# Optimization experiments

Hardware: AMD Instinct MI355X
Metric: run time of the kernel (lower is better)

The kernel has to match this reference:

```python
import jax, jax.numpy as jnp
import numpy as np

B, Q, T, C = 2, 300, 25, 256
NH, NL, NP = 8, 4, 4
DFF = 1024
HD = C // NH
SHAPES = [(128, 128), (64, 64), (32, 32), (16, 16)]  # (H_l, W_l) per level
S = sum(h * w for h, w in SHAPES)
LQ = Q * T


def setup_inputs() -> dict:
    key = jax.random.key(0)
    ks = jax.random.split(key, 16)
    rn = lambda k, shape, s=0.02: jax.random.normal(k, shape, jnp.float32) * s
    starts = np.cumsum([0] + [h * w for h, w in SHAPES[:-1]])
    return {
        "tgt_text": jax.random.normal(ks[0], (B, Q, T, C), jnp.float32),
        "query_pos_text": jax.random.normal(ks[1], (B, Q, T, C), jnp.float32),
        "reference_points": jax.random.uniform(ks[2], (B, LQ, NL, 2), jnp.float32),
        "src": jax.random.normal(ks[3], (B, S, C), jnp.float32),
        "src_spatial_shapes": jnp.array(SHAPES, jnp.int32),
        "level_start_index": jnp.array(starts, jnp.int32),
        "in_proj_w": rn(ks[4], (3 * C, C)), "in_proj_b": jnp.zeros((3 * C,), jnp.float32),
        "out_proj_w": rn(ks[5], (C, C)), "out_proj_b": jnp.zeros((C,), jnp.float32),
        "ln1_g": jnp.ones((C,), jnp.float32), "ln1_b": jnp.zeros((C,), jnp.float32),
        "samp_off_w": rn(ks[6], (NH * NL * NP * 2, C)), "samp_off_b": rn(ks[7], (NH * NL * NP * 2,), 0.5),
        "aw_w": rn(ks[8], (NH * NL * NP, C)), "aw_b": jnp.zeros((NH * NL * NP,), jnp.float32),
        "vp_w": rn(ks[9], (C, C)), "vp_b": jnp.zeros((C,), jnp.float32),
        "op_w": rn(ks[10], (C, C)), "op_b": jnp.zeros((C,), jnp.float32),
        "ln2_g": jnp.ones((C,), jnp.float32), "ln2_b": jnp.zeros((C,), jnp.float32),
        "ffn1_w": rn(ks[11], (DFF, C)), "ffn1_b": jnp.zeros((DFF,), jnp.float32),
        "ffn2_w": rn(ks[12], (C, DFF)), "ffn2_b": jnp.zeros((C,), jnp.float32),
        "ln3_g": jnp.ones((C,), jnp.float32), "ln3_b": jnp.zeros((C,), jnp.float32),
    }


def _ln(x, g, b):
    m = jnp.mean(x, axis=-1, keepdims=True)
    v = jnp.var(x, axis=-1, keepdims=True)
    return (x - m) / jnp.sqrt(v + 1e-5) * g + b


def _self_attn(tgt, pos, in_proj_w, in_proj_b, out_proj_w, out_proj_b):
    # torch nn.MultiheadAttention math: q,k carry pos, v is raw tgt
    qk = (tgt + pos).reshape(B * Q, T, C)
    x = tgt.reshape(B * Q, T, C)
    Wq, Wk, Wv = jnp.split(in_proj_w, 3, axis=0)
    bq, bk, bv = jnp.split(in_proj_b, 3, axis=0)
    heads = lambda t: t.reshape(B * Q, T, NH, HD).transpose(0, 2, 1, 3)
    q = heads(qk @ Wq.T + bq)
    k = heads(qk @ Wk.T + bk)
    v = heads(x @ Wv.T + bv)
    attn = jax.nn.softmax(jnp.einsum("bhqd,bhkd->bhqk", q, k) / jnp.sqrt(jnp.float32(HD)), axis=-1)
    o = jnp.einsum("bhqk,bhkd->bhqd", attn, v).transpose(0, 2, 1, 3).reshape(B * Q, T, C)
    return (o @ out_proj_w.T + out_proj_b).reshape(B, Q, T, C)


def _ms_deform_attn(query, reference_points, src, shapes, samp_off_w, samp_off_b, aw_w, aw_b, vp_w, vp_b, op_w, op_b):
    # query: [B, LQ, C]; src: [B, S, C]
    value = (src @ vp_w.T + vp_b).reshape(B, S, NH, HD)
    off = (query @ samp_off_w.T + samp_off_b).reshape(B, LQ, NH, NL, NP, 2)
    aw = jax.nn.softmax((query @ aw_w.T + aw_b).reshape(B, LQ, NH, NL * NP), axis=-1)
    aw = aw.reshape(B, LQ, NH, NL, NP)
    # normalizer is (W_l, H_l)
    norm = jnp.array([[w, h] for (h, w) in shapes], jnp.float32)
    loc = reference_points[:, :, None, :, None, :] + off / norm[None, None, None, :, None, :]
    starts = np.cumsum([0] + [h * w for h, w in shapes])
    accum = jnp.zeros((B, NH, LQ, HD), jnp.float32)
    for l, (Hl, Wl) in enumerate(shapes):
        vl = value[:, starts[l]:starts[l] + Hl * Wl].transpose(0, 2, 1, 3)  # [B,NH,HW,HD]
        # grid_sample align_corners=False pixel coords
        xl = (loc[:, :, :, l, :, 0] * Wl - 0.5).transpose(0, 2, 1, 3).reshape(B, NH, LQ * NP)
        yl = (loc[:, :, :, l, :, 1] * Hl - 0.5).transpose(0, 2, 1, 3).reshape(B, NH, LQ * NP)
        x0 = jnp.floor(xl); y0 = jnp.floor(yl)
        wx1 = xl - x0; wy1 = yl - y0
        x0i = x0.astype(jnp.int32); y0i = y0.astype(jnp.int32)
        samp = jnp.zeros((B, NH, LQ * NP, HD), jnp.float32)
        for dx, dy, w in ((0, 0, (1 - wx1) * (1 - wy1)), (1, 0, wx1 * (1 - wy1)),
                          (0, 1, (1 - wx1) * wy1), (1, 1, wx1 * wy1)):
            xi = x0i + dx; yi = y0i + dy
            valid = (xi >= 0) & (xi < Wl) & (yi >= 0) & (yi < Hl)
            lin = jnp.clip(yi, 0, Hl - 1) * Wl + jnp.clip(xi, 0, Wl - 1)
            g = jnp.take_along_axis(vl, lin[..., None], axis=2)  # [B,NH,LQ*NP,HD]
            samp = samp + g * (w * valid)[..., None]
        samp = samp.reshape(B, NH, LQ, NP, HD)
        awl = aw[:, :, :, l, :].transpose(0, 2, 1, 3)  # [B,NH,LQ,NP]
        accum = accum + jnp.sum(samp * awl[..., None], axis=3)
    out = accum.transpose(0, 2, 1, 3).reshape(B, LQ, C)
    return out @ op_w.T + op_b


def reference(tgt_text, query_pos_text, reference_points, src, src_spatial_shapes, level_start_index,
              in_proj_w, in_proj_b, out_proj_w, out_proj_b, ln1_g, ln1_b,
              samp_off_w, samp_off_b, aw_w, aw_b, vp_w, vp_b, op_w, op_b, ln2_g, ln2_b,
              ffn1_w, ffn1_b, ffn2_w, ffn2_b, ln3_g, ln3_b):
    shapes = [tuple(int(v) for v in row) for row in np.asarray(src_spatial_shapes)]  # static
    # --- intra-text self-attention ---
    tgt2 = _self_attn(tgt_text, query_pos_text, in_proj_w, in_proj_b, out_proj_w, out_proj_b)
    tgt = _ln(tgt_text + tgt2, ln1_g, ln1_b)
    # --- multi-scale deformable cross-attention ---
    query = (tgt + query_pos_text).reshape(B, LQ, C)
    cross = _ms_deform_attn(query, reference_points, src, shapes,
                            samp_off_w, samp_off_b, aw_w, aw_b, vp_w, vp_b, op_w, op_b)
    tgt = _ln(tgt + cross.reshape(B, Q, T, C), ln2_g, ln2_b)
    # --- FFN ---
    ffn = jax.nn.relu(tgt @ ffn1_w.T + ffn1_b) @ ffn2_w.T + ffn2_b
    return _ln(tgt + ffn, ln3_g, ln3_b)
```

## Files before the change

### kernel.cpp

```cpp
#include <hip/hip_runtime.h>
#include <cstddef>

#define B_ 2
#define Q_ 300
#define T_ 25
#define C_ 256
#define NH_ 8
#define NL_ 4
#define NP_ 4
#define HD_ 32
#define DFF_ 1024
#define LQ_ (Q_ * T_)
#define NTOK_ (B_ * LQ_)
#define S_ 21760
#define BS_ (B_ * S_)

typedef __bf16 bf16x8 __attribute__((ext_vector_type(8)));
typedef float floatx4 __attribute__((ext_vector_type(4)));
typedef unsigned short ushort_t;

__device__ __forceinline__ unsigned pack_bf16(float x, float y) {
    unsigned ux = __float_as_uint(x) + 0x8000u;
    unsigned uy = __float_as_uint(y) + 0x8000u;
    return (ux >> 16) | (uy & 0xFFFF0000u);
}
__device__ __forceinline__ ushort_t f2bf_s(float x) {
    return (ushort_t)((__float_as_uint(x) + 0x8000u) >> 16);
}
__device__ __forceinline__ float bf2f(ushort_t u) {
    return __uint_as_float((unsigned)u << 16);
}

#define WOFF_IP   0
#define WOFF_OUT  196608
#define WOFF_VP   262144
#define WOFF_SO   327680
#define WOFF_AW   393216
#define WOFF_OP   425984
#define WOFF_F1   491520
#define WOFF_F2   753664
#define WTOTAL    1015808

__global__ __launch_bounds__(256) void convw_kernel(
    const float* __restrict__ ipw, const float* __restrict__ outw,
    const float* __restrict__ vpw, const float* __restrict__ sampw,
    const float* __restrict__ aww, const float* __restrict__ opw,
    const float* __restrict__ f1w, const float* __restrict__ f2w,
    ushort_t* __restrict__ dst)
{
    long long g = ((long long)blockIdx.x * 256 + threadIdx.x) * 8;
    if (g >= WTOTAL) return;
    const float* src; long long off;
    if      (g < WOFF_OUT) { src = ipw;   off = WOFF_IP; }
    else if (g < WOFF_VP)  { src = outw;  off = WOFF_OUT; }
    else if (g < WOFF_SO)  { src = vpw;   off = WOFF_VP; }
    else if (g < WOFF_AW)  { src = sampw; off = WOFF_SO; }
    else if (g < WOFF_OP)  { src = aww;   off = WOFF_AW; }
    else if (g < WOFF_F1)  { src = opw;   off = WOFF_OP; }
    else if (g < WOFF_F2)  { src = f1w;   off = WOFF_F1; }
    else                   { src = f2w;   off = WOFF_F2; }
    const float4* s4 = (const float4*)(src + (g - off));
    float4 a = s4[0], b = s4[1];
    uint4 o;
    o.x = pack_bf16(a.x, a.y); o.y = pack_bf16(a.z, a.w);
    o.z = pack_bf16(b.x, b.y); o.w = pack_bf16(b.z, b.w);
    *(uint4*)(dst + g) = o;
}

#define GBN 128
#define GBK 64
#define LDA_S 72

template<int AMODE, int OUTMODE, int GBMT>
__global__ __launch_bounds__(256) void gemm_w(
    const void* __restrict__ Av, const float* __restrict__ A2,
    const ushort_t* __restrict__ W,
    const float* __restrict__ bias, const float* __restrict__ bias2, int N1,
    void* __restrict__ Cv, long long partStride,
    int M, int N, int K, int kChunk, int ldc, int relu)
{
    constexpr int LA = GBMT / 16;
    constexpr int LB = 8;
    constexpr int WM = GBMT / 2;
    constexpr int NI = WM / 16;

    __shared__ unsigned short SH[GBMT * LDA_S + GBN * LDA_S];
    unsigned short* Asl = SH;
    unsigned short* Bsl = SH + GBMT * LDA_S;

    const int m0 = blockIdx.x * GBMT;
    if (m0 >= M) return;
    const int n0 = blockIdx.y * GBN;
    const int z  = blockIdx.z;
    const int kbeg = z * kChunk;
    const int kend = min(K, kbeg + kChunk);

    const int t  = threadIdx.x;
    const int wid  = t >> 6;
    const int lane = t & 63;
    const int wm = (wid >> 1) * WM;
    const int wn = (wid & 1) * 64;
    const int fm = lane & 15;
    const int fq = (lane >> 4) * 8;

    const bool addA2 = (AMODE == 1) && (n0 < N1);

    floatx4 acc[NI][4];
    #pragma unroll
    for (int i = 0; i < NI; ++i)
        #pragma unroll
        for (int j = 0; j < 4; ++j)
            acc[i][j] = (floatx4){0.f, 0.f, 0.f, 0.f};

    float4 pa[LA];
    uint2  pab[LA];
    uint2  pwb[LB];
    const float* Af = (const float*)Av;
    const ushort_t* Ab = (const ushort_t*)Av;

    auto load_tiles = [&](int k0) {
        #pragma unroll
        for (int i = 0; i < LA; ++i) {
            int idx = t + 256 * i;
            int row = idx >> 4;
            int c4  = (idx & 15) * 4;
            int gm = m0 + row;
            if constexpr (AMODE == 2) {
                uint2 v = {0u, 0u};
                if (gm < M) v = *(const uint2*)(Ab + (size_t)gm * K + k0 + c4);
                pab[i] = v;
            } else {
                float4 v = make_float4(0.f, 0.f, 0.f, 0.f);
                if (gm < M) {
                    v = *(const float4*)(Af + (size_t)gm * K + k0 + c4);
                    if constexpr (AMODE == 1) {
                        if (addA2) {
                            float4 v2 = *(const float4*)(A2 + (size_t)gm * K + k0 + c4);
                            v.x += v2.x; v.y += v2.y; v.z += v2.z; v.w += v2.w;
                        }
                    }
                }
                pa[i] = v;
            }
        }
        #pragma unroll
        for (int i = 0; i < LB; ++i) {
            int idx = t + 256 * i;
            int row = idx >> 4;
            int c4  = (idx & 15) * 4;
            pwb[i] = *(const uint2*)(W + (size_t)(n0 + row) * K + k0 + c4);
        }
    };

    load_tiles(kbeg);
    for (int k0 = kbeg; k0 < kend; k0 += GBK) {
        #pragma unroll
        for (int i = 0; i < LA; ++i) {
            int idx = t + 256 * i;
            int row = idx >> 4;
            int c4  = (idx & 15) * 4;
            if constexpr (AMODE == 2) {
                *(uint2*)&Asl[row * LDA_S + c4] = pab[i];
            } else {
                uint2 p;
                p.x = pack_bf16(pa[i].x, pa[i].y);
                p.y = pack_bf16(pa[i].z, pa[i].w);
                *(uint2*)&Asl[row * LDA_S + c4] = p;
            }
        }
        #pragma unroll
        for (int i = 0; i < LB; ++i) {
            int idx = t + 256 * i;
            int row = idx >> 4;
            int c4  = (idx & 15) * 4;
            *(uint2*)&Bsl[row * LDA_S + c4] = pwb[i];
        }
        __syncthreads();
        if (k0 + GBK < kend) load_tiles(k0 + GBK);

        #pragma unroll
        for (int kk = 0; kk < 2; ++kk) {
            bf16x8 af[NI], bfr[4];
            #pragma unroll
            for (int i = 0; i < NI; ++i)
                af[i] = *(const bf16x8*)&Asl[(wm + i * 16 + fm) * LDA_S + kk * 32 + fq];
            #pragma unroll
            for (int j = 0; j < 4; ++j)
                bfr[j] = *(const bf16x8*)&Bsl[(wn + j * 16 + fm) * LDA_S + kk * 32 + fq];

            #pragma unroll
            for (int i = 0; i < NI; ++i)
                #pragma unroll
                for (int j = 0; j < 4; ++j)
                    acc[i][j] = __builtin_amdgcn_mfma_f32_16x16x32_bf16(af[i], bfr[j], acc[i][j], 0, 0, 0);
        }
        __syncthreads();
    }

    float* Cf = (float*)Cv + (long long)z * partStride;
    ushort_t* Cb = (ushort_t*)Cv;
    const int cr = (lane >> 4) * 4;
    const int cc = lane & 15;

    if constexpr (OUTMODE == 0) {
        #pragma unroll
        for (int j = 0; j < 4; ++j) {
            int gn = n0 + wn + j * 16 + cc;
            float bia = 0.f;
            if (z == 0) bia = (bias2 && gn >= N1) ? bias2[gn - N1] : bias[gn];
            #pragma unroll
            for (int i = 0; i < NI; ++i)
                #pragma unroll
                for (int r = 0; r < 4; ++r) {
                    int gm = m0 + wm + i * 16 + cr + r;
                    if (gm < M) {
                        float v = acc[i][j][r] + bia;
                        if (relu) v = fmaxf(v, 0.f);
                        Cf[(size_t)gm * ldc + gn] = v;
                    }
                }
        }
    } else {
        unsigned short* epi = SH + wid * (WM * 64);
        #pragma unroll
        for (int j = 0; j < 4; ++j) {
            int gn = n0 + wn + j * 16 + cc;
            float bia = (bias2 && gn >= N1) ? bias2[gn - N1] : bias[gn];
            #pragma unroll
            for (int i = 0; i < NI; ++i)
                #pragma unroll
                for (int r = 0; r < 4; ++r) {
                    float v = acc[i][j][r] + bia;
                    if (relu) v = fmaxf(v, 0.f);
                    epi[(i * 16 + cr + r) * 64 + j * 16 + cc] = f2bf_s(v);
                }
        }
        #pragma unroll
        for (int pass = 0; pass < WM / 8; ++pass) {
            int lr = pass * 8 + (lane >> 3);
            int gm = m0 + wm + lr;
            uint4 vv = *(const uint4*)&epi[lr * 64 + (lane & 7) * 8];
            if (gm < M) {
                if constexpr (OUTMODE == 1) {
                    *(uint4*)&Cb[(size_t)gm * ldc + n0 + wn + (lane & 7) * 8] = vv;
                } else {
                    int bb = gm >= S_;
                    int s  = gm - bb * S_;
                    int gh = n0 + wn + (lane & 7) * 8;
                    *(uint4*)&Cb[(((size_t)(bb * 8 + (gh >> 5))) * S_ + s) * 32 + (gh & 31)] = vv;
                }
            }
        }
    }
}

__global__ __launch_bounds__(64) void attn_kernel(
    const ushort_t* __restrict__ qkv,
    ushort_t* __restrict__ o)
{
    int sh = blockIdx.x;
    int s = sh >> 3, h = sh & 7;
    __shared__ float qs[T_][HD_], ks[T_][HD_], vs[T_][HD_];
    int t = threadIdx.x;

    for (int idx = t; idx < T_ * HD_; idx += 64) {
        int i = idx >> 5, d = idx & 31;
        size_t base = ((size_t)(s * T_ + i)) * 768 + h * HD_ + d;
        qs[i][d] = bf2f(qkv[base]);
        ks[i][d] = bf2f(qkv[base + 256]);
        vs[i][d] = bf2f(qkv[base + 512]);
    }
    __syncthreads();

    if (t < T_) {
        float sc[T_];
        float mx = -1e30f;
        #pragma unroll
        for (int j = 0; j < T_; ++j) {
            float dot = 0.f;
            #pragma unroll
            for (int d = 0; d < HD_; ++d) dot += qs[t][d] * ks[j][d];
            sc[j] = dot * 0.17677669529663687f;
            mx = fmaxf(mx, sc[j]);
        }
        float sum = 0.f;
        #pragma unroll
        for (int j = 0; j < T_; ++j) { sc[j] = __expf(sc[j] - mx); sum += sc[j]; }
        float inv = 1.f / sum;
        float out[HD_];
        #pragma unroll
        for (int d = 0; d < HD_; ++d) out[d] = 0.f;
        for (int j = 0; j < T_; ++j) {
            float p = sc[j] * inv;
            #pragma unroll
            for (int d = 0; d < HD_; ++d) out[d] += p * vs[j][d];
        }
        size_t ob = ((size_t)(s * T_ + t)) * C_ + h * HD_;
        #pragma unroll
        for (int d = 0; d < HD_; ++d) o[ob + d] = f2bf_s(out[d]);
    }
}

__global__ __launch_bounds__(256) void ln4_kernel(
    const float* x, const float* r,
    int nparts, long long rstride,
    const float* __restrict__ g, const float* __restrict__ b,
    float* out, const float* __restrict__ pos,
    float* qout)
{
    const int wave = threadIdx.x >> 6;
    const int lane = threadIdx.x & 63;
    const int tok = blockIdx.x * 4 + wave;
    const size_t base = (size_t)tok * C_ + lane * 4;

    float4 v = *(const float4*)(x + base);
    for (int p = 0; p < nparts; ++p) {
        float4 rv = *(const float4*)(r + base + (long long)p * rstride);
        v.x += rv.x; v.y += rv.y; v.z += rv.z; v.w += rv.w;
    }
    float s  = v.x + v.y + v.z + v.w;
    float ss = v.x * v.x + v.y * v.y + v.z * v.z + v.w * v.w;
    #pragma unroll
    for (int m = 32; m; m >>= 1) {
        s  += __shfl_xor(s, m);
        ss += __shfl_xor(ss, m);
    }
    float mean = s * (1.f / 256.f);
    float var  = ss * (1.f / 256.f) - mean * mean;
    float rstd = rsqrtf(var + 1e-5f);

    float4 gv = *(const float4*)(g + lane * 4);
    float4 bv = *(const float4*)(b + lane * 4);
    float4 y;
    y.x = (v.x - mean) * rstd * gv.x + bv.x;
    y.y = (v.y - mean) * rstd * gv.y + bv.y;
    y.z = (v.z - mean) * rstd * gv.z + bv.z;
    y.w = (v.w - mean) * rstd * gv.w + bv.w;
    *(float4*)(out + base) = y;
    if (qout) {
        float4 pv = *(const float4*)(pos + base);
        float4 q;
        q.x = y.x + pv.x; q.y = y.y + pv.y; q.z = y.z + pv.z; q.w = y.w + pv.w;
        *(float4*)(qout + base) = q;
    }
}

#define DCHUNK_ 118
__global__ __launch_bounds__(256) void deform_kernel(
    const ushort_t* __restrict__ value,
    const float* __restrict__ d12,
    const float* __restrict__ refpts,
    ushort_t* __restrict__ out)
{
    const int bi    = blockIdx.x;
    const int xcd   = bi & 7;
    const int yy    = bi >> 3;
    const int combo = xcd + 8 * (yy & 1);
    const int chunk = yy >> 1;
    const int h     = combo & 7;
    const int b     = combo >> 3;

    __shared__ float tls[64][60];

    const int tid = threadIdx.x;
    const int t0  = chunk * 64;

    #pragma unroll
    for (int i = 0; i < 2; ++i) {
        int idx  = tid + 256 * i;
        int trow = idx >> 3;
        int c4   = (idx & 7) * 4;
        int tl   = min(t0 + trow, LQ_ - 1);
        float4 v;
        v.x = __builtin_nontemporal_load(d12 + (size_t)(b * LQ_ + tl) * 384 + h * 32 + c4 + 0);
        v.y = __builtin_nontemporal_load(d12 + (size_t)(b * LQ_ + tl) * 384 + h * 32 + c4 + 1);
        v.z = __builtin_nontemporal_load(d12 + (size_t)(b * LQ_ + tl) * 384 + h * 32 + c4 + 2);
        v.w = __builtin_nontemporal_load(d12 + (size_t)(b * LQ_ + tl) * 384 + h * 32 + c4 + 3);
        *(float4*)&tls[trow][c4] = v;
    }
    {
        int trow = tid >> 2;
        int c4   = (tid & 3) * 4;
        int tl   = min(t0 + trow, LQ_ - 1);
        float4 v;
        v.x = __builtin_nontemporal_load(d12 + (size_t)(b * LQ_ + tl) * 384 + 256 + h * 16 + c4 + 0);
        v.y = __builtin_nontemporal_load(d12 + (size_t)(b * LQ_ + tl) * 384 + 256 + h * 16 + c4 + 1);
        v.z = __builtin_nontemporal_load(d12 + (size_t)(b * LQ_ + tl) * 384 + 256 + h * 16 + c4 + 2);
        v.w = __builtin_nontemporal_load(d12 + (size_t)(b * LQ_ + tl) * 384 + 256 + h * 16 + c4 + 3);
        *(float4*)&tls[trow][32 + c4] = v;
    }
    if (tid < 128) {
        int trow = tid >> 1;
        int c4   = (tid & 1) * 4;
        int tl   = min(t0 + trow, LQ_ - 1);
        float4 v;
        v.x = __builtin_nontemporal_load(refpts + (size_t)(b * LQ_ + tl) * 8 + c4 + 0);
        v.y = __builtin_nontemporal_load(refpts + (size_t)(b * LQ_ + tl) * 8 + c4 + 1);
        v.z = __builtin_nontemporal_load(refpts + (size_t)(b * LQ_ + tl) * 8 + c4 + 2);
        v.w = __builtin_nontemporal_load(refpts + (size_t)(b * LQ_ + tl) * 8 + c4 + 3);
        *(float4*)&tls[trow][48 + c4] = v;
    }
    __syncthreads();

    if (tid < 64) {
        float lg[16];
        float mx = -1e30f;
        #pragma unroll
        for (int i = 0; i < 16; ++i) { lg[i] = tls[tid][32 + i]; mx = fmaxf(mx, lg[i]); }
        float sum = 0.f;
        #pragma unroll
        for (int i = 0; i < 16; ++i) { lg[i] = __expf(lg[i] - mx); sum += lg[i]; }
        float inv = 1.f / sum;
        #pragma unroll
        for (int i = 0; i < 16; ++i) tls[tid][32 + i] = lg[i] * inv;
    }
    __syncthreads();

    const int wave = tid >> 6;
    const int lane = tid & 63;
    const int ti   = lane >> 2;
    const int d8   = (lane & 3) * 8;
    const int row  = wave * 16 + ti;

    int tl = t0 + row;
    const bool active = (tl < LQ_);
    tl = min(tl, LQ_ - 1);
    const int tok = b * LQ_ + tl;

    const int HW[4]     = {128, 64, 32, 16};
    const int starts[4] = {0, 16384, 20480, 21504};

    const ushort_t* vplane = value + (size_t)combo * ((size_t)S_ * HD_) + d8;
    const float* trow = tls[row];

    float accv[8];
    #pragma unroll
    for (int i = 0; i < 8; ++i) accv[i] = 0.f;

    #pragma unroll
    for (int l = 0; l < 4; ++l) {
        const int Hl = HW[l], Wl = HW[l];
        float rx = trow[48 + l * 2 + 0];
        float ry = trow[48 + l * 2 + 1];
        const ushort_t* vbase = vplane + (size_t)starts[l] * HD_;
        #pragma unroll
        for (int p = 0; p < 4; ++p) {
            float ox = trow[l * 8 + p * 2 + 0];
            float oy = trow[l * 8 + p * 2 + 1];
            float aww = trow[32 + l * 4 + p];
            float xl = rx * (float)Wl + ox - 0.5f;
            float yl = ry * (float)Hl + oy - 0.5f;
            float x0f = floorf(xl), y0f = floorf(yl);
            int x0 = (int)x0f, y0 = (int)y0f;
            float wx1 = xl - x0f, wy1 = yl - y0f;
            float wx0 = 1.f - wx1, wy0 = 1.f - wy1;

            #pragma unroll
            for (int c = 0; c < 4; ++c) {
                int dx = c & 1, dy = c >> 1;
                int xi = x0 + dx, yi = y0 + dy;
                float w = (dx ? wx1 : wx0) * (dy ? wy1 : wy0);
                bool valid = (xi >= 0) & (xi < Wl) & (yi >= 0) & (yi < Hl);
                int xc = min(max(xi, 0), Wl - 1);
                int yc = min(max(yi, 0), Hl - 1);
                float wc = (valid ? w : 0.f) * aww;
                uint4 raw = *(const uint4*)(vbase + (size_t)(yc * Wl + xc) * HD_);
                accv[0] += __uint_as_float((raw.x & 0xFFFFu) << 16) * wc;
                accv[1] += __uint_as_float(raw.x & 0xFFFF0000u) * wc;
                accv[2] += __uint_as_float((raw.y & 0xFFFFu) << 16) * wc;
                accv[3] += __uint_as_float(raw.y & 0xFFFF0000u) * wc;
                accv[4] += __uint_as_float((raw.z & 0xFFFFu) << 16) * wc;
                accv[5] += __uint_as_float(raw.z & 0xFFFF0000u) * wc;
                accv[6] += __uint_as_float((raw.w & 0xFFFFu) << 16) * wc;
                accv[7] += __uint_as_float(raw.w & 0xFFFF0000u) * wc;
            }
        }
    }
    if (active) {
        uint4 po;
        po.x = pack_bf16(accv[0], accv[1]);
        po.y = pack_bf16(accv[2], accv[3]);
        po.z = pack_bf16(accv[4], accv[5]);
        po.w = pack_bf16(accv[6], accv[7]);
        *(uint4*)(out + (size_t)tok * C_ + h * HD_ + d8) = po;
    }
}

extern "C" void kernel_launch(void* const* d_in, const int* in_sizes, int n_in,
                              void* d_out, int out_size, void* d_ws, size_t ws_size,
                              hipStream_t stream) {
    const float* tgt_text = (const float*)d_in[0];
    const float* pos      = (const float*)d_in[1];
    const float* refpts   = (const float*)d_in[2];
    const float* src      = (const float*)d_in[3];
    const float* in_proj_w  = (const float*)d_in[6];
    const float* in_proj_b  = (const float*)d_in[7];
    const float* out_proj_w = (const float*)d_in[8];
    const float* out_proj_b = (const float*)d_in[9];
    const float* ln1_g = (const float*)d_in[10];
    const float* ln1_b = (const float*)d_in[11];
    const float* samp_off_w = (const float*)d_in[12];
    const float* samp_off_b = (const float*)d_in[13];
    const float* aw_w = (const float*)d_in[14];
    const float* aw_b = (const float*)d_in[15];
    const float* vp_w = (const float*)d_in[16];
    const float* vp_b = (const float*)d_in[17];
    const float* op_w = (const float*)d_in[18];
    const float* op_b = (const float*)d_in[19];
    const float* ln2_g = (const float*)d_in[20];
    const float* ln2_b = (const float*)d_in[21];
    const float* ffn1_w = (const float*)d_in[22];
    const float* ffn1_b = (const float*)d_in[23];
    const float* ffn2_w = (const float*)d_in[24];
    const float* ffn2_b = (const float*)d_in[25];
    const float* ln3_g = (const float*)d_in[26];
    const float* ln3_b = (const float*)d_in[27];

    const long long NC = (long long)NTOK_ * C_;
    float* ws = (float*)d_ws;
    float* A    = ws;
    float* Bq   = ws + NC;
    float* Creg = ws + 2 * NC;
    float* D12  = Creg + (long long)NTOK_ * DFF_;
    float* E    = D12 + (long long)NTOK_ * 384;
    float* F    = E + NC;
    ushort_t* wb = (ushort_t*)(F + NC);

    ushort_t* qkv  = (ushort_t*)Creg;
    ushort_t* valt = (ushort_t*)Creg + (size_t)NTOK_ * 768;

    const int MB64P  = 240;
    const int MB128P = 120;
    const int MBV64  = BS_ / 64;

    convw_kernel<<<496, 256, 0, stream>>>(in_proj_w, out_proj_w, vp_w, samp_off_w,
                                          aw_w, op_w, ffn1_w, ffn2_w, wb);
    gemm_w<1, 1, 64><<<dim3(MB64P, 6, 1), 256, 0, stream>>>(tgt_text, pos, wb + WOFF_IP,
        in_proj_b, nullptr, 512, qkv, 0, NTOK_, 768, 256, 256, 768, 0);
    gemm_w<0, 2, 64><<<dim3(MBV64, 2, 1), 256, 0, stream>>>(src, nullptr, wb + WOFF_VP,
        vp_b, nullptr, 0, valt, 0, BS_, 256, 256, 256, 0, 0);
    attn_kernel<<<B_ * Q_ * NH_, 64, 0, stream>>>(qkv, (ushort_t*)E);
    gemm_w<2, 0, 64><<<dim3(MB64P, 2, 2), 256, 0, stream>>>(E, nullptr, wb + WOFF_OUT,
        out_proj_b, nullptr, 0, ws, NC, NTOK_, 256, 256, 128, 256, 0);
    ln4_kernel<<<NTOK_ / 4, 256, 0, stream>>>(tgt_text, ws, 2, NC,
                                              ln1_g, ln1_b, A, pos, Bq);
    gemm_w<0, 0, 64><<<dim3(MB64P, 3, 1), 256, 0, stream>>>(Bq, nullptr, wb + WOFF_SO,
        samp_off_b, aw_b, 256, D12, 0, NTOK_, 384, 256, 256, 384, 0);
    deform_kernel<<<8 * 2 * DCHUNK_, 256, 0, stream>>>(valt, D12, refpts, (ushort_t*)E);
    gemm_w<2, 0, 64><<<dim3(MB64P, 2, 2), 256, 0, stream>>>(E, nullptr, wb + WOFF_OP,
        op_b, nullptr, 0, Creg, NC, NTOK_, 256, 256, 128, 256, 0);
    ln4_kernel<<<NTOK_ / 4, 256, 0, stream>>>(A, Creg, 2, NC,
                                              ln2_g, ln2_b, A, nullptr, nullptr);
    gemm_w<0, 1, 128><<<dim3(MB128P, 8, 1), 256, 0, stream>>>(A, nullptr, wb + WOFF_F1,
        ffn1_b, nullptr, 0, Creg, 0, NTOK_, DFF_, 256, 256, DFF_, 1);
    gemm_w<2, 0, 128><<<dim3(MB128P, 2, 2), 256, 0, stream>>>(Creg, nullptr, wb + WOFF_F2,
        ffn2_b, nullptr, 0, E, NC, NTOK_, 256, 1024, 512, 256, 0);
    ln4_kernel<<<NTOK_ / 4, 256, 0, stream>>>(A, E, 2, NC,
                                              ln3_g, ln3_b, (float*)d_out, nullptr, nullptr);
}
```

Before: 406.3 us.

## Batch deform gather loads per level and drop split-K for small projections

After: 384.2 us. 5.4% less time.

```diff
diff --git a/kernel.cpp b/kernel.cpp
--- a/kernel.cpp
+++ b/kernel.cpp
@@ -346,7 +346,7 @@
 }
 
 #define DCHUNK_ 118
-__global__ __launch_bounds__(256) void deform_kernel(
+__global__ __launch_bounds__(256, 4) void deform_kernel(
     const ushort_t* __restrict__ value,
     const float* __restrict__ d12,
     const float* __restrict__ refpts,
@@ -368,37 +368,37 @@
     #pragma unroll
     for (int i = 0; i < 2; ++i) {
         int idx  = tid + 256 * i;
-        int trow = idx >> 3;
+        int trw  = idx >> 3;
         int c4   = (idx & 7) * 4;
-        int tl   = min(t0 + trow, LQ_ - 1);
+        int tl   = min(t0 + trw, LQ_ - 1);
         float4 v;
         v.x = __builtin_nontemporal_load(d12 + (size_t)(b * LQ_ + tl) * 384 + h * 32 + c4 + 0);
         v.y = __builtin_nontemporal_load(d12 + (size_t)(b * LQ_ + tl) * 384 + h * 32 + c4 + 1);
         v.z = __builtin_nontemporal_load(d12 + (size_t)(b * LQ_ + tl) * 384 + h * 32 + c4 + 2);
         v.w = __builtin_nontemporal_load(d12 + (size_t)(b * LQ_ + tl) * 384 + h * 32 + c4 + 3);
-        *(float4*)&tls[trow][c4] = v;
+        *(float4*)&tls[trw][c4] = v;
     }
     {
-        int trow = tid >> 2;
-        int c4   = (tid & 3) * 4;
-        int tl   = min(t0 + trow, LQ_ - 1);
+        int trw = tid >> 2;
+        int c4  = (tid & 3) * 4;
+        int tl  = min(t0 + trw, LQ_ - 1);
         float4 v;
         v.x = __builtin_nontemporal_load(d12 + (size_t)(b * LQ_ + tl) * 384 + 256 + h * 16 + c4 + 0);
         v.y = __builtin_nontemporal_load(d12 + (size_t)(b * LQ_ + tl) * 384 + 256 + h * 16 + c4 + 1);
         v.z = __builtin_nontemporal_load(d12 + (size_t)(b * LQ_ + tl) * 384 + 256 + h * 16 + c4 + 2);
         v.w = __builtin_nontemporal_load(d12 + (size_t)(b * LQ_ + tl) * 384 + 256 + h * 16 + c4 + 3);
-        *(float4*)&tls[trow][32 + c4] = v;
+        *(float4*)&tls[trw][32 + c4] = v;
     }
     if (tid < 128) {
-        int trow = tid >> 1;
-        int c4   = (tid & 1) * 4;
-        int tl   = min(t0 + trow, LQ_ - 1);
+        int trw = tid >> 1;
+        int c4  = (tid & 1) * 4;
+        int tl  = min(t0 + trw, LQ_ - 1);
         float4 v;
         v.x = __builtin_nontemporal_load(refpts + (size_t)(b * LQ_ + tl) * 8 + c4 + 0);
         v.y = __builtin_nontemporal_load(refpts + (size_t)(b * LQ_ + tl) * 8 + c4 + 1);
         v.z = __builtin_nontemporal_load(refpts + (size_t)(b * LQ_ + tl) * 8 + c4 + 2);
         v.w = __builtin_nontemporal_load(refpts + (size_t)(b * LQ_ + tl) * 8 + c4 + 3);
-        *(float4*)&tls[trow][48 + c4] = v;
+        *(float4*)&tls[trw][48 + c4] = v;
     }
     __syncthreads();
 
@@ -443,6 +443,9 @@
         float rx = trow[48 + l * 2 + 0];
         float ry = trow[48 + l * 2 + 1];
         const ushort_t* vbase = vplane + (size_t)starts[l] * HD_;
+
+        int   voff[16];
+        float wgt[16];
         #pragma unroll
         for (int p = 0; p < 4; ++p) {
             float ox = trow[l * 8 + p * 2 + 0];
@@ -454,7 +457,6 @@
             int x0 = (int)x0f, y0 = (int)y0f;
             float wx1 = xl - x0f, wy1 = yl - y0f;
             float wx0 = 1.f - wx1, wy0 = 1.f - wy1;
-
             #pragma unroll
             for (int c = 0; c < 4; ++c) {
                 int dx = c & 1, dy = c >> 1;
@@ -463,17 +465,25 @@
                 bool valid = (xi >= 0) & (xi < Wl) & (yi >= 0) & (yi < Hl);
                 int xc = min(max(xi, 0), Wl - 1);
                 int yc = min(max(yi, 0), Hl - 1);
-                float wc = (valid ? w : 0.f) * aww;
-                uint4 raw = *(const uint4*)(vbase + (size_t)(yc * Wl + xc) * HD_);
-                accv[0] += __uint_as_float((raw.x & 0xFFFFu) << 16) * wc;
-                accv[1] += __uint_as_float(raw.x & 0xFFFF0000u) * wc;
-                accv[2] += __uint_as_float((raw.y & 0xFFFFu) << 16) * wc;
-                accv[3] += __uint_as_float(raw.y & 0xFFFF0000u) * wc;
-                accv[4] += __uint_as_float((raw.z & 0xFFFFu) << 16) * wc;
-                accv[5] += __uint_as_float(raw.z & 0xFFFF0000u) * wc;
-                accv[6] += __uint_as_float((raw.w & 0xFFFFu) << 16) * wc;
-                accv[7] += __uint_as_float(raw.w & 0xFFFF0000u) * wc;
+                voff[p * 4 + c] = yc * Wl + xc;
+                wgt[p * 4 + c]  = (valid ? w : 0.f) * aww;
             }
+        }
+        uint4 raw[16];
+        #pragma unroll
+        for (int i = 0; i < 16; ++i)
+            raw[i] = *(const uint4*)(vbase + (size_t)voff[i] * HD_);
+        #pragma unroll
+        for (int i = 0; i < 16; ++i) {
+            float wc = wgt[i];
+            accv[0] += __uint_as_float((raw[i].x & 0xFFFFu) << 16) * wc;
+            accv[1] += __uint_as_float(raw[i].x & 0xFFFF0000u) * wc;
+            accv[2] += __uint_as_float((raw[i].y & 0xFFFFu) << 16) * wc;
+            accv[3] += __uint_as_float(raw[i].y & 0xFFFF0000u) * wc;
+            accv[4] += __uint_as_float((raw[i].z & 0xFFFFu) << 16) * wc;
+            accv[5] += __uint_as_float(raw[i].z & 0xFFFF0000u) * wc;
+            accv[6] += __uint_as_float((raw[i].w & 0xFFFFu) << 16) * wc;
+            accv[7] += __uint_as_float(raw[i].w & 0xFFFF0000u) * wc;
         }
     }
     if (active) {
@@ -540,16 +550,16 @@
     gemm_w<0, 2, 64><<<dim3(MBV64, 2, 1), 256, 0, stream>>>(src, nullptr, wb + WOFF_VP,
         vp_b, nullptr, 0, valt, 0, BS_, 256, 256, 256, 0, 0);
     attn_kernel<<<B_ * Q_ * NH_, 64, 0, stream>>>(qkv, (ushort_t*)E);
-    gemm_w<2, 0, 64><<<dim3(MB64P, 2, 2), 256, 0, stream>>>(E, nullptr, wb + WOFF_OUT,
-        out_proj_b, nullptr, 0, ws, NC, NTOK_, 256, 256, 128, 256, 0);
-    ln4_kernel<<<NTOK_ / 4, 256, 0, stream>>>(tgt_text, ws, 2, NC,
+    gemm_w<2, 0, 64><<<dim3(MB64P, 2, 1), 256, 0, stream>>>(E, nullptr, wb + WOFF_OUT,
+        out_proj_b, nullptr, 0, F, 0, NTOK_, 256, 256, 256, 256, 0);
+    ln4_kernel<<<NTOK_ / 4, 256, 0, stream>>>(tgt_text, F, 1, 0,
                                               ln1_g, ln1_b, A, pos, Bq);
     gemm_w<0, 0, 64><<<dim3(MB64P, 3, 1), 256, 0, stream>>>(Bq, nullptr, wb + WOFF_SO,
         samp_off_b, aw_b, 256, D12, 0, NTOK_, 384, 256, 256, 384, 0);
     deform_kernel<<<8 * 2 * DCHUNK_, 256, 0, stream>>>(valt, D12, refpts, (ushort_t*)E);
-    gemm_w<2, 0, 64><<<dim3(MB64P, 2, 2), 256, 0, stream>>>(E, nullptr, wb + WOFF_OP,
-        op_b, nullptr, 0, Creg, NC, NTOK_, 256, 256, 128, 256, 0);
-    ln4_kernel<<<NTOK_ / 4, 256, 0, stream>>>(A, Creg, 2, NC,
+    gemm_w<2, 0, 64><<<dim3(MB64P, 2, 1), 256, 0, stream>>>(E, nullptr, wb + WOFF_OP,
+        op_b, nullptr, 0, F, 0, NTOK_, 256, 256, 256, 256, 0);
+    ln4_kernel<<<NTOK_ / 4, 256, 0, stream>>>(A, F, 1, 0,
                                               ln2_g, ln2_b, A, nullptr, nullptr);
     gemm_w<0, 1, 128><<<dim3(MB128P, 8, 1), 256, 0, stream>>>(A, nullptr, wb + WOFF_F1,
         ffn1_b, nullptr, 0, Creg, 0, NTOK_, DFF_, 256, 256, DFF_, 1);
```
